# Kernel optimization log

Measured on AMD Instinct MI355X. Metric: run time of the kernel, lower is better.

## Reference

```python
import jax, jax.numpy as jnp
import numpy as np

B, S, D = 2, 4096, 512
H = 8
W = 512            # local attention window size
HD = D // H        # head dim
NC = S // W        # number of chunks
HALF = W // 2      # symmetric half-window


def setup_inputs() -> dict:
    key = jax.random.key(0)
    ks = jax.random.split(key, 12)
    s = 1.0 / np.sqrt(D)
    return {
        "val": jax.random.normal(ks[0], (B, S, D), jnp.float32),
        "Wq": jax.random.normal(ks[1], (D, D), jnp.float32) * s,
        "bq": jnp.zeros((D,), jnp.float32),
        "Wk": jax.random.normal(ks[2], (D, D), jnp.float32) * s,
        "bk": jnp.zeros((D,), jnp.float32),
        "Wv": jax.random.normal(ks[3], (D, D), jnp.float32) * s,
        "bv": jnp.zeros((D,), jnp.float32),
        "Wo": jax.random.normal(ks[4], (D, D), jnp.float32) * s,
        "bo": jnp.zeros((D,), jnp.float32),
        "gamma": jnp.ones((D,), jnp.float32),
        "beta": jnp.zeros((D,), jnp.float32),
    }


def _heads(x):
    # [B,S,D] -> [B,H,S,HD]
    return x.reshape(B, S, H, HD).transpose(0, 2, 1, 3)


def _gather_neighbors(x):
    # x: [B,H,S,HD] -> [B,H,NC,3W,HD] (prev | cur | next chunk, zero-padded at ends)
    xp = jnp.pad(x, ((0, 0), (0, 0), (W, W), (0, 0)))
    xc = xp.reshape(B, H, NC + 2, W, HD)
    return jnp.concatenate([xc[:, :, :-2], xc[:, :, 1:-1], xc[:, :, 2:]], axis=3)


def _local_attention(x, Wq, bq, Wk, bk, Wv, bv, Wo, bo):
    q = _heads(x @ Wq + bq)
    k = _heads(x @ Wk + bk)
    v = _heads(x @ Wv + bv)

    qc = q.reshape(B, H, NC, W, HD)            # chunked queries
    kn = _gather_neighbors(k)                  # [B,H,NC,3W,HD]
    vn = _gather_neighbors(v)

    scale = 1.0 / np.sqrt(HD)
    scores = jnp.einsum("bhcqd,bhckd->bhcqk", qc, kn) * scale  # [B,H,NC,W,3W]

    # banded mask: key relative position in [-HALF, HALF], and key index in [0,S)
    qi = jnp.arange(W)[:, None]
    kj = jnp.arange(3 * W)[None, :]
    band = jnp.abs(kj - W - qi) <= HALF                          # [W,3W]
    key_pos = (jnp.arange(NC)[:, None, None] - 1) * W + kj[None]  # [NC,1,3W]
    valid = (key_pos >= 0) & (key_pos < S)                       # [NC,1,3W]
    mask = band[None] & valid                                    # [NC,W,3W]

    scores = jnp.where(mask[None, None], scores, jnp.float32(-1e9))
    p = jax.nn.softmax(scores, axis=-1)
    o = jnp.einsum("bhcqk,bhckd->bhcqd", p, vn)                  # [B,H,NC,W,HD]
    o = o.reshape(B, H, S, HD).transpose(0, 2, 1, 3).reshape(B, S, D)
    return o @ Wo + bo


def _layer_norm(x, gamma, beta, eps=1e-5):
    mu = jnp.mean(x, axis=-1, keepdims=True)
    var = jnp.mean(jnp.square(x - mu), axis=-1, keepdims=True)
    return (x - mu) * jax.lax.rsqrt(var + eps) * gamma + beta


def reference(val, Wq, bq, Wk, bk, Wv, bv, Wo, bo, gamma, beta):
    attn_out = _local_attention(val, Wq, bq, Wk, bk, Wv, bv, Wo, bo)
    return _layer_norm(val + attn_out, gamma, beta)
```

## Files before the change

### kernel.cpp

```cpp
#include <hip/hip_runtime.h>
#include <hip/hip_bf16.h>

#define BATCH 2
#define SEQ   4096
#define DIM   512
#define NHEAD 8
#define HDIM  64
#define ROWS  (BATCH*SEQ)

typedef float  fx4   __attribute__((ext_vector_type(4)));
typedef __bf16 bf16x8 __attribute__((ext_vector_type(8)));
typedef unsigned short ushort_t;
typedef unsigned short usx4 __attribute__((ext_vector_type(4)));
typedef unsigned short usx8 __attribute__((ext_vector_type(8)));

static __device__ __forceinline__ float b2f(ushort_t v) {
    union { unsigned int u; float f; } c; c.u = ((unsigned int)v) << 16; return c.f;
}
static __device__ __forceinline__ ushort_t f2b(float f) {
    union { float f; unsigned int u; } c; c.f = f;
    unsigned int u = c.u;
    unsigned int r = (u + 0x7FFFu + ((u >> 16) & 1u)) >> 16;
    return (ushort_t)r;
}
static __device__ __forceinline__ void gload16(const ushort_t* g, ushort_t* l) {
    __builtin_amdgcn_global_load_lds(
        (const __attribute__((address_space(1))) unsigned int*)g,
        (__attribute__((address_space(3))) unsigned int*)l, 16, 0, 0);
}

__global__ __launch_bounds__(256) void prep_kernel(
    const float* __restrict__ val, ushort_t* __restrict__ xb,
    const float* __restrict__ W0, const float* __restrict__ W1,
    const float* __restrict__ W2, const float* __restrict__ W3,
    ushort_t* __restrict__ T0, ushort_t* __restrict__ T1,
    ushort_t* __restrict__ T2, ushort_t* __restrict__ T3) {

    const int tid = threadIdx.x;
    if (blockIdx.y >= 4) {
        const int bid = blockIdx.x + 64 * (blockIdx.y - 4);
        const int stride = 256 * 256 * 4;
        for (int i = (bid * 256 + tid) * 4; i < ROWS * 512; i += stride) {
            fx4 v = *(const fx4*)(val + i);
            usx4 o; o.x = f2b(v.x); o.y = f2b(v.y); o.z = f2b(v.z); o.w = f2b(v.w);
            *(usx4*)(xb + i) = o;
        }
        return;
    }
    const float* W; ushort_t* WT;
    switch (blockIdx.y) {
        case 0: W = W0; WT = T0; break;
        case 1: W = W1; WT = T1; break;
        case 2: W = W2; WT = T2; break;
        default: W = W3; WT = T3; break;
    }
    __shared__ float tile[64][65];
    int r0 = (blockIdx.x & 7) * 64;
    int c0 = (blockIdx.x >> 3) * 64;
    for (int idx = tid; idx < 4096; idx += 256) {
        int rr = idx >> 6, cc = idx & 63;
        tile[rr][cc] = W[(c0 + rr) * 512 + (r0 + cc)];
    }
    __syncthreads();
    for (int idx = tid; idx < 4096; idx += 256) {
        int rr = idx >> 6, cc = idx & 63;
        WT[(size_t)(r0 + rr) * 512 + (c0 + cc)] = f2b(tile[cc][rr]);
    }
}

__global__ __launch_bounds__(256) void gemm128_kernel(
    const ushort_t* __restrict__ A,
    const ushort_t* __restrict__ BT0, const ushort_t* __restrict__ BT1, const ushort_t* __restrict__ BT2,
    const float* __restrict__ b0, const float* __restrict__ b1, const float* __restrict__ b2,
    ushort_t* __restrict__ C0, ushort_t* __restrict__ C1, ushort_t* __restrict__ C2) {

    const ushort_t* BT; const float* bias; ushort_t* C;
    if (blockIdx.z == 0)      { BT = BT0; bias = b0; C = C0; }
    else if (blockIdx.z == 1) { BT = BT1; bias = b1; C = C1; }
    else                      { BT = BT2; bias = b2; C = C2; }

    __shared__ ushort_t As[128 * 32];
    __shared__ ushort_t Bs[128 * 32];

    const int tid  = threadIdx.x;
    const int wave = tid >> 6;
    const int lane = tid & 63;
    const int lm   = lane & 15;
    const int quad = lane >> 4;
    const int wm   = wave >> 1;
    const int wn   = wave & 1;

    const int m0t = blockIdx.x * 128;
    const int n0t = blockIdx.y * 128;

    const int srow = tid >> 2, sgc = tid & 3;
    const ushort_t* ga0 = A  + (size_t)(m0t + srow) * 512 + sgc * 8;
    const ushort_t* ga1 = ga0 + (size_t)64 * 512;
    const ushort_t* gb0 = BT + (size_t)(n0t + srow) * 512 + sgc * 8;
    const ushort_t* gb1 = gb0 + (size_t)64 * 512;
    ushort_t* la0 = As + tid * 8;
    ushort_t* la1 = As + (tid + 256) * 8;
    ushort_t* lb0 = Bs + tid * 8;
    ushort_t* lb1 = Bs + (tid + 256) * 8;

    const int aoff = (wm * 64 + lm) * 32 + quad * 8;
    const int boff = (wn * 64 + lm) * 32 + quad * 8;

    fx4 acc[4][4];
    #pragma unroll
    for (int i = 0; i < 4; ++i)
        #pragma unroll
        for (int j = 0; j < 4; ++j) acc[i][j] = 0;

    for (int k0 = 0; k0 < 512; k0 += 32) {
        __syncthreads();
        gload16(ga0 + k0, la0);
        gload16(ga1 + k0, la1);
        gload16(gb0 + k0, lb0);
        gload16(gb1 + k0, lb1);
        __syncthreads();

        bf16x8 af[4], bfr[4];
        #pragma unroll
        for (int ms = 0; ms < 4; ++ms) af[ms]  = *(const bf16x8*)&As[aoff + ms * 512];
        #pragma unroll
        for (int ns = 0; ns < 4; ++ns) bfr[ns] = *(const bf16x8*)&Bs[boff + ns * 512];
        #pragma unroll
        for (int ms = 0; ms < 4; ++ms)
            #pragma unroll
            for (int ns = 0; ns < 4; ++ns)
                acc[ms][ns] = __builtin_amdgcn_mfma_f32_16x16x32_bf16(af[ms], bfr[ns], acc[ms][ns], 0, 0, 0);
    }

    const int crow0 = m0t + wm * 64 + quad * 4;
    const int ccol0 = n0t + wn * 64 + lm;

    if (blockIdx.z == 2) {
        #pragma unroll
        for (int ns = 0; ns < 4; ++ns) {
            int col = ccol0 + ns * 16;
            int h = col >> 6, d = col & 63;
            float bv = bias[col];
            #pragma unroll
            for (int ms = 0; ms < 4; ++ms) {
                int m = crow0 + ms * 16;
                int bb = m >> 12, s0 = m & 4095;
                usx4 o;
                o.x = f2b(acc[ms][ns][0] + bv); o.y = f2b(acc[ms][ns][1] + bv);
                o.z = f2b(acc[ms][ns][2] + bv); o.w = f2b(acc[ms][ns][3] + bv);
                *(usx4*)(C + (((size_t)(bb * 8 + h) * 64 + d) * 4096 + s0)) = o;
            }
        }
    } else {
        #pragma unroll
        for (int ns = 0; ns < 4; ++ns) {
            int col = ccol0 + ns * 16;
            float bv = bias[col];
            #pragma unroll
            for (int ms = 0; ms < 4; ++ms) {
                #pragma unroll
                for (int r = 0; r < 4; ++r) {
                    C[(size_t)(crow0 + ms * 16 + r) * 512 + col] = f2b(acc[ms][ns][r] + bv);
                }
            }
        }
    }
}

__global__ __launch_bounds__(256, 4) void attn_mfma_kernel(
    const ushort_t* __restrict__ Qb, const ushort_t* __restrict__ Kb,
    const ushort_t* __restrict__ Vt, ushort_t* __restrict__ Ob) {

    __shared__ ushort_t Klds[64 * 64];
    __shared__ ushort_t Vlds[64 * 64];
    __shared__ ushort_t Plds[4 * 16 * 72];

    const int tid  = threadIdx.x;
    const int wave = tid >> 6;
    const int lane = tid & 63;
    const int lm   = lane & 15;
    const int quad = lane >> 4;

    const int wg = blockIdx.x;
    const int l  = (wg & 7) * 128 + (wg >> 3);
    const int bh = l >> 6;
    const int b = bh >> 3, h = bh & 7;
    const int q0 = (l & 63) * 64;
    const int qw = q0 + wave * 16;

    const ushort_t* qp = Qb + ((size_t)(b * SEQ + qw + lm)) * 512 + h * 64 + quad * 8;
    bf16x8 qf0 = *(const bf16x8*)qp;
    bf16x8 qf1 = *(const bf16x8*)(qp + 32);

    int koff[2][4], voff[2][4];
    #pragma unroll
    for (int ks = 0; ks < 2; ++ks) {
        #pragma unroll
        for (int tn = 0; tn < 4; ++tn) {
            int key = tn * 16 + lm;
            koff[ks][tn] = key * 64 + (((ks * 4 + quad) ^ (key & 7)) * 8);
            int d = tn * 16 + lm;
            voff[ks][tn] = d * 64 + (((ks * 4 + quad) ^ (d & 7)) * 8);
        }
    }
    ushort_t* Pw = Plds + wave * (16 * 72);
    const int pwbase = lm * 72 + quad * 4;
    const int prbase = lm * 72 + quad * 8;

    const int skey = tid >> 3;
    const int sdg  = tid & 7;
    const size_t kgbase = ((size_t)b * SEQ) * 512 + h * 64 + sdg * 8;
    const size_t vgbase = ((size_t)bh * 64) * 4096 + sdg * 8;
    const int l0 = skey * 64 + ((sdg ^ (skey & 7)) * 8);
    const int l1 = l0 + 32 * 64;

    const int klo = (q0 >= 256) ? 0 : ((256 - q0) >> 6);
    const int khi = min(8, (4288 - q0) >> 6);

    bf16x8 onesf;
    {
        __bf16 o = (lm == 0) ? (__bf16)1.0f : (__bf16)0.0f;
        #pragma unroll
        for (int j = 0; j < 8; ++j) onesf[j] = o;
    }

    fx4 oacc[4];
    oacc[0] = 0; oacc[1] = 0; oacc[2] = 0; oacc[3] = 0;
    fx4 lacc = 0;

    usx8 kn0, kn1, vn0, vn1;
    {
        int ts = q0 - 256 + klo * 64;
        kn0 = *(const usx8*)(Kb + kgbase + (size_t)(ts + skey) * 512);
        kn1 = *(const usx8*)(Kb + kgbase + (size_t)(ts + skey + 32) * 512);
        vn0 = *(const usx8*)(Vt + vgbase + (size_t)skey * 4096 + ts);
        vn1 = *(const usx8*)(Vt + vgbase + (size_t)(skey + 32) * 4096 + ts);
    }

    for (int kt = klo; kt <= khi; ++kt) {
        const int ts = q0 - 256 + kt * 64;
        __syncthreads();
        *(usx8*)&Klds[l0] = kn0;
        *(usx8*)&Klds[l1] = kn1;
        *(usx8*)&Vlds[l0] = vn0;
        *(usx8*)&Vlds[l1] = vn1;
        __syncthreads();

        if (kt < khi) {
            int t2 = ts + 64;
            kn0 = *(const usx8*)(Kb + kgbase + (size_t)(t2 + skey) * 512);
            kn1 = *(const usx8*)(Kb + kgbase + (size_t)(t2 + skey + 32) * 512);
            vn0 = *(const usx8*)(Vt + vgbase + (size_t)skey * 4096 + t2);
            vn1 = *(const usx8*)(Vt + vgbase + (size_t)(skey + 32) * 4096 + t2);
        }

        bf16x8 kf[2][4];
        #pragma unroll
        for (int ks = 0; ks < 2; ++ks)
            #pragma unroll
            for (int tn = 0; tn < 4; ++tn)
                kf[ks][tn] = *(const bf16x8*)&Klds[koff[ks][tn]];
        fx4 sacc[4];
        sacc[0] = 0; sacc[1] = 0; sacc[2] = 0; sacc[3] = 0;
        #pragma unroll
        for (int ks = 0; ks < 2; ++ks) {
            bf16x8 q8 = ks ? qf1 : qf0;
            #pragma unroll
            for (int tn = 0; tn < 4; ++tn)
                sacc[tn] = __builtin_amdgcn_mfma_f32_16x16x32_bf16(kf[ks][tn], q8, sacc[tn], 0, 0, 0);
        }

        const bool edge = (ts < qw - 241) || (ts > qw + 193);
        const int qg = qw + lm;
        #pragma unroll
        for (int tn = 0; tn < 4; ++tn) {
            usx4 pk;
            #pragma unroll
            for (int r = 0; r < 4; ++r) {
                float p = __expf(sacc[tn][r] * 0.125f);
                if (edge) {
                    int dlt = (ts + tn * 16 + quad * 4 + r) - qg;
                    p = (dlt <= 256 && dlt >= -256) ? p : 0.0f;
                }
                pk[r] = f2b(p);
            }
            *(usx4*)&Pw[pwbase + tn * 16] = pk;
        }

        bf16x8 vf[2][4];
        #pragma unroll
        for (int ks = 0; ks < 2; ++ks)
            #pragma unroll
            for (int tn = 0; tn < 4; ++tn)
                vf[ks][tn] = *(const bf16x8*)&Vlds[voff[ks][tn]];
        #pragma unroll
        for (int ks = 0; ks < 2; ++ks) {
            bf16x8 ap = *(const bf16x8*)&Pw[prbase + ks * 32];
            lacc = __builtin_amdgcn_mfma_f32_16x16x32_bf16(ap, onesf, lacc, 0, 0, 0);
            #pragma unroll
            for (int tn = 0; tn < 4; ++tn)
                oacc[tn] = __builtin_amdgcn_mfma_f32_16x16x32_bf16(ap, vf[ks][tn], oacc[tn], 0, 0, 0);
        }
    }

    float linv[4];
    #pragma unroll
    for (int r = 0; r < 4; ++r) {
        float lv = __shfl(lacc[r], (lane & 48));
        linv[r] = 1.0f / lv;
    }
    ushort_t* ob = Ob + ((size_t)(b * SEQ + qw + quad * 4)) * 512 + h * 64 + lm;
    #pragma unroll
    for (int tn = 0; tn < 4; ++tn)
        #pragma unroll
        for (int r = 0; r < 4; ++r)
            ob[(size_t)r * 512 + tn * 16] = f2b(oacc[tn][r] * linv[r]);
}

__global__ __launch_bounds__(256) void ln_kernel(
    const ushort_t* __restrict__ xb, const ushort_t* __restrict__ ob,
    const float* __restrict__ gamma, const float* __restrict__ beta,
    float* __restrict__ out) {

    int row  = blockIdx.x * 4 + (threadIdx.x >> 6);
    int lane = threadIdx.x & 63;

    const ushort_t* xp = xb + (size_t)row * 512 + lane * 8;
    const ushort_t* op = ob + (size_t)row * 512 + lane * 8;

    usx4 xa = ((const usx4*)xp)[0];
    usx4 xc = ((const usx4*)xp)[1];
    usx4 oa = ((const usx4*)op)[0];
    usx4 oc = ((const usx4*)op)[1];
    fx4 va, vb;
    va.x = b2f(xa.x) + b2f(oa.x); va.y = b2f(xa.y) + b2f(oa.y);
    va.z = b2f(xa.z) + b2f(oa.z); va.w = b2f(xa.w) + b2f(oa.w);
    vb.x = b2f(xc.x) + b2f(oc.x); vb.y = b2f(xc.y) + b2f(oc.y);
    vb.z = b2f(xc.z) + b2f(oc.z); vb.w = b2f(xc.w) + b2f(oc.w);

    float s = va.x + va.y + va.z + va.w + vb.x + vb.y + vb.z + vb.w;
    #pragma unroll
    for (int m = 32; m > 0; m >>= 1) s += __shfl_xor(s, m);
    float mu = s * (1.0f / 512.0f);

    fx4 da = va - mu;
    fx4 db = vb - mu;
    float ss = da.x*da.x + da.y*da.y + da.z*da.z + da.w*da.w
             + db.x*db.x + db.y*db.y + db.z*db.z + db.w*db.w;
    #pragma unroll
    for (int m = 32; m > 0; m >>= 1) ss += __shfl_xor(ss, m);
    float rstd = rsqrtf(ss * (1.0f / 512.0f) + 1e-5f);

    const fx4* gp = (const fx4*)(gamma + lane * 8);
    const fx4* bp = (const fx4*)(beta  + lane * 8);
    fx4 g0 = gp[0], g1 = gp[1], b0 = bp[0], b1 = bp[1];

    float* outp = out + (size_t)row * 512 + lane * 8;
    fx4 r0 = da * rstd * g0 + b0;
    fx4 r1 = db * rstd * g1 + b1;
    ((fx4*)outp)[0] = r0;
    ((fx4*)outp)[1] = r1;
}

extern "C" void kernel_launch(void* const* d_in, const int* in_sizes, int n_in,
                              void* d_out, int out_size, void* d_ws, size_t ws_size,
                              hipStream_t stream) {
    const float* val   = (const float*)d_in[0];
    const float* Wq    = (const float*)d_in[1];
    const float* bq    = (const float*)d_in[2];
    const float* Wk    = (const float*)d_in[3];
    const float* bk    = (const float*)d_in[4];
    const float* Wv    = (const float*)d_in[5];
    const float* bv    = (const float*)d_in[6];
    const float* Wo    = (const float*)d_in[7];
    const float* bo    = (const float*)d_in[8];
    const float* gamma = (const float*)d_in[9];
    const float* beta  = (const float*)d_in[10];
    float* out = (float*)d_out;

    char* w = (char*)d_ws;
    ushort_t* xb    = (ushort_t*)w; w += (size_t)ROWS * 512 * 2;
    ushort_t* WqT   = (ushort_t*)w; w += 512 * 512 * 2;
    ushort_t* WkT   = (ushort_t*)w; w += 512 * 512 * 2;
    ushort_t* WvT   = (ushort_t*)w; w += 512 * 512 * 2;
    ushort_t* WoT   = (ushort_t*)w; w += 512 * 512 * 2;
    ushort_t* Qb    = (ushort_t*)w; w += (size_t)ROWS * 512 * 2;
    ushort_t* Kb    = (ushort_t*)w; w += (size_t)ROWS * 512 * 2;
    ushort_t* Vtb   = (ushort_t*)w; w += (size_t)ROWS * 512 * 2;
    ushort_t* attnb = (ushort_t*)w; w += (size_t)ROWS * 512 * 2;
    ushort_t* obuf  = (ushort_t*)w; w += (size_t)ROWS * 512 * 2;

    prep_kernel<<<dim3(64, 8), 256, 0, stream>>>(
        val, xb, Wq, Wk, Wv, Wo, WqT, WkT, WvT, WoT);

    gemm128_kernel<<<dim3(ROWS / 128, 4, 3), 256, 0, stream>>>(
        xb, WqT, WkT, WvT, bq, bk, bv, Qb, Kb, Vtb);

    attn_mfma_kernel<<<1024, 256, 0, stream>>>(Qb, Kb, Vtb, attnb);

    gemm128_kernel<<<dim3(ROWS / 128, 4, 1), 256, 0, stream>>>(
        attnb, WoT, WoT, WoT, bo, bo, bo, obuf, obuf, obuf);

    ln_kernel<<<ROWS / 4, 256, 0, stream>>>(xb, obuf, gamma, beta, out);
}
```

Before: 160.7 us.

## Double attention query tile per block to reuse K/V tiles across 128 queries

Each attention workgroup now handles 128 queries instead of 64, with every wave processing two 16-row query groups against the same K/V LDS tiles. This halves the grid and roughly halves the global K/V loads and LDS staging per query, amortising the barriers. In exchange the key range per block grows (10 instead of 9 tiles, with more masked waste), register pressure rises, occupancy is lowered via launch bounds, and only 512 blocks remain to fill the GPU.

```diff
diff --git a/kernel.cpp b/kernel.cpp
--- a/kernel.cpp
+++ b/kernel.cpp
@@ -167,13 +167,13 @@
     }
 }
 
-__global__ __launch_bounds__(256, 4) void attn_mfma_kernel(
+__global__ __launch_bounds__(256, 2) void attn_mfma_kernel(
     const ushort_t* __restrict__ Qb, const ushort_t* __restrict__ Kb,
     const ushort_t* __restrict__ Vt, ushort_t* __restrict__ Ob) {
 
     __shared__ ushort_t Klds[64 * 64];
     __shared__ ushort_t Vlds[64 * 64];
-    __shared__ ushort_t Plds[4 * 16 * 72];
+    __shared__ ushort_t Plds[4 * 32 * 72];
 
     const int tid  = threadIdx.x;
     const int wave = tid >> 6;
@@ -182,15 +182,19 @@
     const int quad = lane >> 4;
 
     const int wg = blockIdx.x;
-    const int l  = (wg & 7) * 128 + (wg >> 3);
-    const int bh = l >> 6;
+    const int l  = (wg & 7) * 64 + (wg >> 3);
+    const int bh = l >> 5;
     const int b = bh >> 3, h = bh & 7;
-    const int q0 = (l & 63) * 64;
-    const int qw = q0 + wave * 16;
-
-    const ushort_t* qp = Qb + ((size_t)(b * SEQ + qw + lm)) * 512 + h * 64 + quad * 8;
-    bf16x8 qf0 = *(const bf16x8*)qp;
-    bf16x8 qf1 = *(const bf16x8*)(qp + 32);
+    const int q0 = (l & 31) * 128;
+    const int qw = q0 + wave * 32;
+
+    bf16x8 qf[2][2];
+    #pragma unroll
+    for (int qg = 0; qg < 2; ++qg) {
+        const ushort_t* qp = Qb + ((size_t)(b * SEQ + qw + qg * 16 + lm)) * 512 + h * 64 + quad * 8;
+        qf[qg][0] = *(const bf16x8*)qp;
+        qf[qg][1] = *(const bf16x8*)(qp + 32);
+    }
 
     int koff[2][4], voff[2][4];
     #pragma unroll
@@ -203,9 +207,7 @@
             voff[ks][tn] = d * 64 + (((ks * 4 + quad) ^ (d & 7)) * 8);
         }
     }
-    ushort_t* Pw = Plds + wave * (16 * 72);
-    const int pwbase = lm * 72 + quad * 4;
-    const int prbase = lm * 72 + quad * 8;
+    ushort_t* Pw = Plds + wave * (32 * 72);
 
     const int skey = tid >> 3;
     const int sdg  = tid & 7;
@@ -215,7 +217,7 @@
     const int l1 = l0 + 32 * 64;
 
     const int klo = (q0 >= 256) ? 0 : ((256 - q0) >> 6);
-    const int khi = min(8, (4288 - q0) >> 6);
+    const int khi = min(9, (4351 - q0) >> 6);
 
     bf16x8 onesf;
     {
@@ -224,9 +226,13 @@
         for (int j = 0; j < 8; ++j) onesf[j] = o;
     }
 
-    fx4 oacc[4];
-    oacc[0] = 0; oacc[1] = 0; oacc[2] = 0; oacc[3] = 0;
-    fx4 lacc = 0;
+    fx4 oacc[2][4];
+    #pragma unroll
+    for (int qg = 0; qg < 2; ++qg)
+        #pragma unroll
+        for (int tn = 0; tn < 4; ++tn) oacc[qg][tn] = 0;
+    fx4 lacc[2];
+    lacc[0] = 0; lacc[1] = 0;
 
     usx8 kn0, kn1, vn0, vn1;
     {
@@ -260,31 +266,35 @@
             #pragma unroll
             for (int tn = 0; tn < 4; ++tn)
                 kf[ks][tn] = *(const bf16x8*)&Klds[koff[ks][tn]];
-        fx4 sacc[4];
-        sacc[0] = 0; sacc[1] = 0; sacc[2] = 0; sacc[3] = 0;
-        #pragma unroll
-        for (int ks = 0; ks < 2; ++ks) {
-            bf16x8 q8 = ks ? qf1 : qf0;
-            #pragma unroll
-            for (int tn = 0; tn < 4; ++tn)
-                sacc[tn] = __builtin_amdgcn_mfma_f32_16x16x32_bf16(kf[ks][tn], q8, sacc[tn], 0, 0, 0);
-        }
-
-        const bool edge = (ts < qw - 241) || (ts > qw + 193);
-        const int qg = qw + lm;
-        #pragma unroll
-        for (int tn = 0; tn < 4; ++tn) {
-            usx4 pk;
-            #pragma unroll
-            for (int r = 0; r < 4; ++r) {
-                float p = __expf(sacc[tn][r] * 0.125f);
-                if (edge) {
-                    int dlt = (ts + tn * 16 + quad * 4 + r) - qg;
-                    p = (dlt <= 256 && dlt >= -256) ? p : 0.0f;
+
+        #pragma unroll
+        for (int qg = 0; qg < 2; ++qg) {
+            fx4 sacc[4];
+            sacc[0] = 0; sacc[1] = 0; sacc[2] = 0; sacc[3] = 0;
+            #pragma unroll
+            for (int ks = 0; ks < 2; ++ks) {
+                bf16x8 q8 = qf[qg][ks];
+                #pragma unroll
+                for (int tn = 0; tn < 4; ++tn)
+                    sacc[tn] = __builtin_amdgcn_mfma_f32_16x16x32_bf16(kf[ks][tn], q8, sacc[tn], 0, 0, 0);
+            }
+            const int qbase = qw + qg * 16;
+            const bool edge = (ts < qbase - 241) || (ts > qbase + 193);
+            const int qg_q = qbase + lm;
+            #pragma unroll
+            for (int tn = 0; tn < 4; ++tn) {
+                usx4 pk;
+                #pragma unroll
+                for (int r = 0; r < 4; ++r) {
+                    float p = __expf(sacc[tn][r] * 0.125f);
+                    if (edge) {
+                        int dlt = (ts + tn * 16 + quad * 4 + r) - qg_q;
+                        p = (dlt <= 256 && dlt >= -256) ? p : 0.0f;
+                    }
+                    pk[r] = f2b(p);
                 }
-                pk[r] = f2b(p);
+                *(usx4*)&Pw[(qg * 16 + lm) * 72 + tn * 16 + quad * 4] = pk;
             }
-            *(usx4*)&Pw[pwbase + tn * 16] = pk;
         }
 
         bf16x8 vf[2][4];
@@ -294,27 +304,33 @@
             for (int tn = 0; tn < 4; ++tn)
                 vf[ks][tn] = *(const bf16x8*)&Vlds[voff[ks][tn]];
         #pragma unroll
-        for (int ks = 0; ks < 2; ++ks) {
-            bf16x8 ap = *(const bf16x8*)&Pw[prbase + ks * 32];
-            lacc = __builtin_amdgcn_mfma_f32_16x16x32_bf16(ap, onesf, lacc, 0, 0, 0);
-            #pragma unroll
-            for (int tn = 0; tn < 4; ++tn)
-                oacc[tn] = __builtin_amdgcn_mfma_f32_16x16x32_bf16(ap, vf[ks][tn], oacc[tn], 0, 0, 0);
-        }
-    }
-
-    float linv[4];
-    #pragma unroll
-    for (int r = 0; r < 4; ++r) {
-        float lv = __shfl(lacc[r], (lane & 48));
-        linv[r] = 1.0f / lv;
-    }
-    ushort_t* ob = Ob + ((size_t)(b * SEQ + qw + quad * 4)) * 512 + h * 64 + lm;
-    #pragma unroll
-    for (int tn = 0; tn < 4; ++tn)
-        #pragma unroll
-        for (int r = 0; r < 4; ++r)
-            ob[(size_t)r * 512 + tn * 16] = f2b(oacc[tn][r] * linv[r]);
+        for (int qg = 0; qg < 2; ++qg) {
+            #pragma unroll
+            for (int ks = 0; ks < 2; ++ks) {
+                bf16x8 ap = *(const bf16x8*)&Pw[(qg * 16 + lm) * 72 + ks * 32 + quad * 8];
+                lacc[qg] = __builtin_amdgcn_mfma_f32_16x16x32_bf16(ap, onesf, lacc[qg], 0, 0, 0);
+                #pragma unroll
+                for (int tn = 0; tn < 4; ++tn)
+                    oacc[qg][tn] = __builtin_amdgcn_mfma_f32_16x16x32_bf16(ap, vf[ks][tn], oacc[qg][tn], 0, 0, 0);
+            }
+        }
+    }
+
+    #pragma unroll
+    for (int qg = 0; qg < 2; ++qg) {
+        float linv[4];
+        #pragma unroll
+        for (int r = 0; r < 4; ++r) {
+            float lv = __shfl(lacc[qg][r], (lane & 48));
+            linv[r] = 1.0f / lv;
+        }
+        ushort_t* ob = Ob + ((size_t)(b * SEQ + qw + qg * 16 + quad * 4)) * 512 + h * 64 + lm;
+        #pragma unroll
+        for (int tn = 0; tn < 4; ++tn)
+            #pragma unroll
+            for (int r = 0; r < 4; ++r)
+                ob[(size_t)r * 512 + tn * 16] = f2b(oacc[qg][tn][r] * linv[r]);
+    }
 }
 
 __global__ __launch_bounds__(256) void ln_kernel(
@@ -396,7 +412,7 @@
     gemm128_kernel<<<dim3(ROWS / 128, 4, 3), 256, 0, stream>>>(
         xb, WqT, WkT, WvT, bq, bk, bv, Qb, Kb, Vtb);
 
-    attn_mfma_kernel<<<1024, 256, 0, stream>>>(Qb, Kb, Vtb, attnb);
+    attn_mfma_kernel<<<512, 256, 0, stream>>>(Qb, Kb, Vtb, attnb);
 
     gemm128_kernel<<<dim3(ROWS / 128, 4, 1), 256, 0, stream>>>(
         attnb, WoT, WoT, WoT, bo, bo, bo, obuf, obuf, obuf);
```

New measurement: 162.2 us. No clear change (+0.9%).
